# Kernel tuning notes

Measured on AMD Instinct MI355X. Metric: run time of the kernel, lower is better.

Reference implementation:

```python
import jax, jax.numpy as jnp
import numpy as np

T = 1024      # tokens
H = 2048      # hidden_size
I = 1408      # moe_intermediate_size
E = 16        # n_routed_experts
K = 6         # num_experts_per_tok
SI = I * 2    # shared experts intermediate (n_shared_experts=2)


def setup_inputs() -> dict:
    key = jax.random.key(0)
    ks = jax.random.split(key, 8)
    s = 0.02
    return {
        "x": jax.random.normal(ks[0], (T, H), jnp.float32),
        "gate_w": jax.random.normal(ks[1], (E, H), jnp.float32) * s,
        "w_gate": jax.random.normal(ks[2], (E, I, H), jnp.float32) * s,
        "w_up": jax.random.normal(ks[3], (E, I, H), jnp.float32) * s,
        "w_down": jax.random.normal(ks[4], (E, H, I), jnp.float32) * s,
        "sw_gate": jax.random.normal(ks[5], (SI, H), jnp.float32) * s,
        "sw_up": jax.random.normal(ks[6], (SI, H), jnp.float32) * s,
        "sw_down": jax.random.normal(ks[7], (H, SI), jnp.float32) * s,
    }


def reference(x, gate_w, w_gate, w_up, w_down, sw_gate, sw_up, sw_down):
    t = x.shape[0]
    # ---- router: softmax over experts, top-k, renormalize (norm_topk_prob) ----
    logits = x @ gate_w.T                                   # [T, E]
    probs = jax.nn.softmax(logits.astype(jnp.float32), axis=-1)
    topw, topi = jax.lax.top_k(probs, K)                    # [T, K]
    topw = topw / jnp.sum(topw, axis=-1, keepdims=True)
    # per-token per-expert combine weight (0 for unselected experts)
    comb = jnp.zeros((t, E), probs.dtype).at[
        jnp.arange(t)[:, None], topi
    ].add(topw)                                             # [T, E]

    # ---- routed experts: SwiGLU MLP per expert, weighted combine ----
    g = jnp.einsum('th,eih->tei', x, w_gate)                # [T, E, I]
    u = jnp.einsum('th,eih->tei', x, w_up)                  # [T, E, I]
    h = jax.nn.silu(g) * u                                  # [T, E, I]
    routed = jnp.einsum('te,tei,ehi->th', comb, h, w_down)  # [T, H]

    # ---- shared experts (always-on SwiGLU MLP) ----
    shared = (jax.nn.silu(x @ sw_gate.T) * (x @ sw_up.T)) @ sw_down.T  # [T, H]

    return routed + shared
```

## Files before the change

### kernel.cpp

```cpp
#include <hip/hip_runtime.h>
#include <stdint.h>

#define T_TOK 1024
#define H_DIM 2048
#define I_DIM 1408
#define E_NUM 16
#define K_TOP 6
#define SI_DIM 2816
#define PADCAP 8192

typedef __attribute__((ext_vector_type(8))) short short8;
typedef __attribute__((ext_vector_type(8))) unsigned short ushort8;
typedef __attribute__((ext_vector_type(4))) float f32x4;

__device__ __forceinline__ unsigned short f2b(float f) {
    unsigned u = __float_as_uint(f);
    u += 0x7fffu + ((u >> 16) & 1u);
    return (unsigned short)(u >> 16);
}
__device__ __forceinline__ float b2f(unsigned short s) {
    return __uint_as_float((unsigned)s << 16);
}

__device__ __forceinline__ int xcd_swizzle(int bid, int nwg) {
    const int q = nwg >> 3, r = nwg & 7;
    const int xcd = bid & 7, k = bid >> 3;
    const int base = (xcd < r) ? xcd * (q + 1) : r * (q + 1) + (xcd - r) * q;
    return base + k;
}

__global__ __launch_bounds__(256) void router_kernel(
    const float* __restrict__ x, const float* __restrict__ gw,
    float* __restrict__ topw, int* __restrict__ eidx, int* __restrict__ slotarr,
    int* __restrict__ counts)
{
    const int t = blockIdx.x, tid = threadIdx.x;
    const int lane = tid & 63, wave = tid >> 6;
    float part[E_NUM];
#pragma unroll
    for (int e = 0; e < E_NUM; ++e) part[e] = 0.f;
    const float* xr = x + (size_t)t * H_DIM;
    for (int i = tid; i < H_DIM; i += 256) {
        float xv = xr[i];
#pragma unroll
        for (int e = 0; e < E_NUM; ++e) part[e] += xv * gw[e * H_DIM + i];
    }
    __shared__ float red[4][E_NUM];
#pragma unroll
    for (int e = 0; e < E_NUM; ++e) {
        float v = part[e];
        for (int off = 32; off; off >>= 1) v += __shfl_down(v, off);
        if (lane == 0) red[wave][e] = v;
    }
    __syncthreads();
    if (tid == 0) {
        float logits[E_NUM];
#pragma unroll
        for (int e = 0; e < E_NUM; ++e)
            logits[e] = red[0][e] + red[1][e] + red[2][e] + red[3][e];
        int sel[K_TOP]; float selv[K_TOP];
        unsigned used = 0;
        for (int k = 0; k < K_TOP; ++k) {
            int best = 0; float bv = -1e30f;
            for (int e = 0; e < E_NUM; ++e)
                if (!((used >> e) & 1u) && logits[e] > bv) { bv = logits[e]; best = e; }
            used |= 1u << best; sel[k] = best; selv[k] = bv;
        }
        float mx = selv[0], s = 0.f, w[K_TOP];
        for (int k = 0; k < K_TOP; ++k) { w[k] = expf(selv[k] - mx); s += w[k]; }
        float inv = 1.f / s;
        for (int k = 0; k < K_TOP; ++k) {
            int slot = atomicAdd(&counts[sel[k]], 1);
            topw[t * K_TOP + k] = w[k] * inv;
            eidx[t * K_TOP + k] = sel[k];
            slotarr[t * K_TOP + k] = slot;
        }
    }
}

__global__ void zero_counts_kernel(int* counts) {
    if (threadIdx.x < E_NUM) counts[threadIdx.x] = 0;
}

__global__ void prefix_kernel(const int* __restrict__ counts, int* __restrict__ offs) {
    if (threadIdx.x == 0) {
        int o = 0;
        for (int e = 0; e < E_NUM; ++e) { offs[e] = o; o += (counts[e] + 127) & ~127; }
        offs[E_NUM] = o;
    }
}

__global__ __launch_bounds__(256) void gather_rows_kernel(
    const float* __restrict__ x, const int* __restrict__ eidx,
    const int* __restrict__ slotarr, const int* __restrict__ offs,
    ushort* __restrict__ Xg)
{
    const int b = blockIdx.x;
    const int t = b / K_TOP;
    const int e = eidx[b], s = slotarr[b];
    const size_t row = (size_t)offs[e] + (size_t)s;
    const float* src = x + (size_t)t * H_DIM;
    ushort* dst = Xg + row * H_DIM;
    const int i = threadIdx.x * 8;
    float4 f0 = *(const float4*)(src + i);
    float4 f1 = *(const float4*)(src + i + 4);
    ushort8 v;
    v[0] = f2b(f0.x); v[1] = f2b(f0.y); v[2] = f2b(f0.z); v[3] = f2b(f0.w);
    v[4] = f2b(f1.x); v[5] = f2b(f1.y); v[6] = f2b(f1.z); v[7] = f2b(f1.w);
    *(ushort8*)(dst + i) = v;
}

__global__ __launch_bounds__(256) void cvt_rows_kernel(
    const float* __restrict__ x, ushort* __restrict__ Xb)
{
    const size_t row = blockIdx.x;
    const float* src = x + row * H_DIM;
    ushort* dst = Xb + row * H_DIM;
    const int i = threadIdx.x * 8;
    float4 f0 = *(const float4*)(src + i);
    float4 f1 = *(const float4*)(src + i + 4);
    ushort8 v;
    v[0] = f2b(f0.x); v[1] = f2b(f0.y); v[2] = f2b(f0.z); v[3] = f2b(f0.w);
    v[4] = f2b(f1.x); v[5] = f2b(f1.y); v[6] = f2b(f1.z); v[7] = f2b(f1.w);
    *(ushort8*)(dst + i) = v;
}

template<int STORE_F32>
__global__ __launch_bounds__(256) void gemm_bt_kernel(
    const ushort* __restrict__ Abase,
    const float* __restrict__ B1, const float* __restrict__ B2,
    void* __restrict__ C1, void* __restrict__ C2,
    const int* __restrict__ counts, const int* __restrict__ offs,
    int Mconst, int nNT, int totNT, int nMT, int K, long strideB, int ldc)
{
    __shared__ short Alds[2][128 * 64];
    __shared__ short Blds[2][128 * 64];

    const int work = xcd_swizzle(blockIdx.x, gridDim.x);
    const int perE = totNT * nMT;
    const int e = work / perE;
    int rem = work - e * perE;
    int nt = rem / nMT;
    const int mt = rem - nt * nMT;

    int M = Mconst, rowbase = 0;
    if (counts) { M = counts[e]; rowbase = offs[e]; }
    const int row0 = mt * 128;
    if (row0 >= M) return;

    const float* Bsel = B1;
    void* Csel = C1;
    if (nt >= nNT) { Bsel = B2; Csel = C2; nt -= nNT; }
    const int n0 = nt * 128;
    const float* __restrict__ B = Bsel + (size_t)e * (size_t)strideB;
    const short* __restrict__ A = (const short*)Abase + (size_t)(rowbase + row0) * K;

    const int tid = threadIdx.x;
    const int lane = tid & 63;
    const int wave = tid >> 6;
    const int wm = wave & 1, wn = wave >> 1;
    const int l15 = lane & 15, lhi = lane >> 4;

    const int r0 = tid >> 3, sl = tid & 7;
    const int swsl = sl ^ (r0 & 7);
    const int ldsoff = (r0 << 6) + (swsl << 3);
    const short* Ag = A + (size_t)r0 * K + (sl << 3);
    const float* Bg = B + (size_t)(n0 + r0) * K + (sl << 3);

    f32x4 acc[4][4];
#pragma unroll
    for (int m = 0; m < 4; ++m)
#pragma unroll
        for (int n = 0; n < 4; ++n) acc[m][n] = (f32x4){0.f, 0.f, 0.f, 0.f};

    short8 a_reg[4];
    float4 b_reg[4][2];

    auto issue = [&](int k0) {
#pragma unroll
        for (int i = 0; i < 4; ++i) {
            a_reg[i] = *(const short8*)(Ag + (size_t)(i << 5) * K + k0);
            const float* bp = Bg + (size_t)(i << 5) * K + k0;
            b_reg[i][0] = *(const float4*)bp;
            b_reg[i][1] = *(const float4*)(bp + 4);
        }
    };
    auto store_lds = [&](int p) {
#pragma unroll
        for (int i = 0; i < 4; ++i) {
            const int off = ldsoff + (i << 11);
            *(short8*)&Alds[p][off] = a_reg[i];
            short8 v;
            v[0] = (short)f2b(b_reg[i][0].x); v[1] = (short)f2b(b_reg[i][0].y);
            v[2] = (short)f2b(b_reg[i][0].z); v[3] = (short)f2b(b_reg[i][0].w);
            v[4] = (short)f2b(b_reg[i][1].x); v[5] = (short)f2b(b_reg[i][1].y);
            v[6] = (short)f2b(b_reg[i][1].z); v[7] = (short)f2b(b_reg[i][1].w);
            *(short8*)&Blds[p][off] = v;
        }
    };

    const int nK = K >> 6;
    issue(0);
    store_lds(0);
    __syncthreads();

    int p = 0;
    for (int t = 0; t < nK; ++t) {
        const bool more = (t + 1 < nK);
        if (more) issue((t + 1) << 6);
#pragma unroll
        for (int kk = 0; kk < 2; ++kk) {
            short8 af[4], bfr[4];
            const int kb = (kk << 2) + lhi;
#pragma unroll
            for (int m = 0; m < 4; ++m) {
                const int rA = (wm << 6) + (m << 4) + l15;
                af[m] = *(const short8*)&Alds[p][(rA << 6) + ((kb ^ (rA & 7)) << 3)];
            }
#pragma unroll
            for (int n = 0; n < 4; ++n) {
                const int rB = (wn << 6) + (n << 4) + l15;
                bfr[n] = *(const short8*)&Blds[p][(rB << 6) + ((kb ^ (rB & 7)) << 3)];
            }
#pragma unroll
            for (int m = 0; m < 4; ++m)
#pragma unroll
                for (int n = 0; n < 4; ++n)
                    acc[m][n] = __builtin_amdgcn_mfma_f32_16x16x32_bf16(
                        af[m], bfr[n], acc[m][n], 0, 0, 0);
        }
        if (more) store_lds(p ^ 1);
        __syncthreads();
        p ^= 1;
    }

    const size_t cbase_col = (size_t)n0 + (wn << 6) + l15;
#pragma unroll
    for (int m = 0; m < 4; ++m) {
        const int rloc = (wm << 6) + (m << 4) + (lhi << 2);
#pragma unroll
        for (int j = 0; j < 4; ++j) {
            const int crow = row0 + rloc + j;
            if (crow >= M) continue;
            const size_t co = (size_t)(rowbase + crow) * ldc + cbase_col;
            if (STORE_F32) {
                float* C = (float*)Csel;
#pragma unroll
                for (int n = 0; n < 4; ++n) C[co + (n << 4)] = acc[m][n][j];
            } else {
                ushort* C = (ushort*)Csel;
#pragma unroll
                for (int n = 0; n < 4; ++n) C[co + (n << 4)] = f2b(acc[m][n][j]);
            }
        }
    }
}

__global__ __launch_bounds__(256) void silu_rows_kernel(
    const ushort* __restrict__ G, const ushort* __restrict__ U,
    ushort* __restrict__ Hh, const int* __restrict__ eidx,
    const int* __restrict__ slotarr, const int* __restrict__ offs, int rowlen)
{
    size_t row;
    if (eidx) {
        const int b = blockIdx.x;
        row = (size_t)offs[eidx[b]] + (size_t)slotarr[b];
    } else {
        row = blockIdx.x;
    }
    const ushort* g = G + row * rowlen;
    const ushort* u = U + row * rowlen;
    ushort* h = Hh + row * rowlen;
    for (int i = threadIdx.x * 8; i < rowlen; i += 2048) {
        ushort8 gv = *(const ushort8*)(g + i);
        ushort8 uv = *(const ushort8*)(u + i);
        ushort8 hv;
#pragma unroll
        for (int j = 0; j < 8; ++j) {
            float gf = b2f(gv[j]);
            float uf = b2f(uv[j]);
            float sf = gf / (1.f + expf(-gf));
            hv[j] = f2b(sf * uf);
        }
        *(ushort8*)(h + i) = hv;
    }
}

__global__ __launch_bounds__(256) void combine_kernel(
    float* __restrict__ out, const ushort* __restrict__ Y,
    const float* __restrict__ topw, const int* __restrict__ eidx,
    const int* __restrict__ slotarr, const int* __restrict__ offs)
{
    const int t = blockIdx.x;
    const int i = threadIdx.x * 8;
    float* o = out + (size_t)t * H_DIM;
    float acc[8];
    float4 o0 = *(const float4*)(o + i);
    float4 o1 = *(const float4*)(o + i + 4);
    acc[0] = o0.x; acc[1] = o0.y; acc[2] = o0.z; acc[3] = o0.w;
    acc[4] = o1.x; acc[5] = o1.y; acc[6] = o1.z; acc[7] = o1.w;
#pragma unroll
    for (int k = 0; k < K_TOP; ++k) {
        const float w = topw[t * K_TOP + k];
        const size_t row = (size_t)offs[eidx[t * K_TOP + k]] + (size_t)slotarr[t * K_TOP + k];
        ushort8 v = *(const ushort8*)(Y + row * H_DIM + i);
#pragma unroll
        for (int j = 0; j < 8; ++j) acc[j] += w * b2f(v[j]);
    }
    o0.x = acc[0]; o0.y = acc[1]; o0.z = acc[2]; o0.w = acc[3];
    o1.x = acc[4]; o1.y = acc[5]; o1.z = acc[6]; o1.w = acc[7];
    *(float4*)(o + i) = o0;
    *(float4*)(o + i + 4) = o1;
}

extern "C" void kernel_launch(void* const* d_in, const int* in_sizes, int n_in,
                              void* d_out, int out_size, void* d_ws, size_t ws_size,
                              hipStream_t stream) {
    const float* x       = (const float*)d_in[0];
    const float* gate_w  = (const float*)d_in[1];
    const float* w_gate  = (const float*)d_in[2];
    const float* w_up    = (const float*)d_in[3];
    const float* w_down  = (const float*)d_in[4];
    const float* sw_gate = (const float*)d_in[5];
    const float* sw_up   = (const float*)d_in[6];
    const float* sw_down = (const float*)d_in[7];
    float* out = (float*)d_out;

    char* p = (char*)d_ws;
    auto take = [&](size_t b) { char* r = p; p += (b + 255) & ~(size_t)255; return r; };
    int*    counts = (int*)take(E_NUM * 4);
    int*    offs   = (int*)take((E_NUM + 1) * 4);
    float*  topw   = (float*)take((size_t)T_TOK * K_TOP * 4);
    int*    eidx   = (int*)take((size_t)T_TOK * K_TOP * 4);
    int*    slot   = (int*)take((size_t)T_TOK * K_TOP * 4);
    ushort* Xg     = (ushort*)take((size_t)PADCAP * H_DIM * 2);
    ushort* G      = (ushort*)take((size_t)PADCAP * I_DIM * 2);
    ushort* U      = (ushort*)take((size_t)PADCAP * I_DIM * 2);
    ushort* Hr     = (ushort*)take((size_t)PADCAP * I_DIM * 2);
    ushort* Xb     = (ushort*)take((size_t)T_TOK * H_DIM * 2);
    ushort* Gs     = (ushort*)take((size_t)T_TOK * SI_DIM * 2);
    ushort* Us     = (ushort*)take((size_t)T_TOK * SI_DIM * 2);
    ushort* Hs     = (ushort*)take((size_t)T_TOK * SI_DIM * 2);

    zero_counts_kernel<<<1, 64, 0, stream>>>(counts);
    router_kernel<<<T_TOK, 256, 0, stream>>>(x, gate_w, topw, eidx, slot, counts);
    prefix_kernel<<<1, 64, 0, stream>>>(counts, offs);
    gather_rows_kernel<<<T_TOK * K_TOP, 256, 0, stream>>>(x, eidx, slot, offs, Xg);
    cvt_rows_kernel<<<T_TOK, 256, 0, stream>>>(x, Xb);

    gemm_bt_kernel<0><<<E_NUM * 22 * 8, 256, 0, stream>>>(
        Xg, w_gate, w_up, G, U, counts, offs,
        0, 11, 22, 8, H_DIM, (long)I_DIM * H_DIM, I_DIM);
    silu_rows_kernel<<<T_TOK * K_TOP, 256, 0, stream>>>(G, U, Hr, eidx, slot, offs, I_DIM);
    gemm_bt_kernel<0><<<E_NUM * 16 * 8, 256, 0, stream>>>(
        Hr, w_down, nullptr, Xg, nullptr, counts, offs,
        0, 16, 16, 8, I_DIM, (long)H_DIM * I_DIM, H_DIM);

    gemm_bt_kernel<0><<<44 * 8, 256, 0, stream>>>(
        Xb, sw_gate, sw_up, Gs, Us, nullptr, nullptr,
        T_TOK, 22, 44, 8, H_DIM, 0, SI_DIM);
    silu_rows_kernel<<<T_TOK, 256, 0, stream>>>(Gs, Us, Hs, nullptr, nullptr, nullptr, SI_DIM);
    gemm_bt_kernel<1><<<16 * 8, 256, 0, stream>>>(
        Hs, sw_down, nullptr, out, nullptr, nullptr, nullptr,
        T_TOK, 16, 16, 8, SI_DIM, 0, H_DIM);

    combine_kernel<<<T_TOK, 256, 0, stream>>>(out, Xg, topw, eidx, slot, offs);
}
```

Baseline: 511.3 us.

## Load GEMM tiles directly into LDS and convert fp32 weights at fragment read

Replaces the register-staged, double-buffered global-to-LDS copy with direct global_load_lds transfers into a single LDS buffer. The B operand is now kept in LDS as fp32 and converted to bf16 with packed cvt instructions when fragments are read, rather than being converted before the LDS store. This is meant to cut VGPR pressure and the instructions spent staging data through registers. The cost is losing overlap between loads and MFMA, since each k-step waits on barriers around the load, and B now uses twice the LDS bandwidth and is converted redundantly by every wave that reads it.

New measurement: 553.8 us, median of 2. 8.3% more time.

```diff
diff --git a/kernel.cpp b/kernel.cpp
--- a/kernel.cpp
+++ b/kernel.cpp
@@ -20,6 +20,18 @@
 }
 __device__ __forceinline__ float b2f(unsigned short s) {
     return __uint_as_float((unsigned)s << 16);
+}
+
+__device__ __forceinline__ unsigned cvt_pk2(float a, float b) {
+    unsigned r;
+    asm("v_cvt_pk_bf16_f32 %0, %1, %2" : "=v"(r) : "v"(a), "v"(b));
+    return r;
+}
+
+typedef __attribute__((address_space(1))) const unsigned int as1_uint;
+typedef __attribute__((address_space(3))) unsigned int as3_uint;
+__device__ __forceinline__ void gload16(const void* g, void* l) {
+    __builtin_amdgcn_global_load_lds((as1_uint*)g, (as3_uint*)l, 16, 0, 0);
 }
 
 __device__ __forceinline__ int xcd_swizzle(int bid, int nwg) {
@@ -133,8 +145,8 @@
     const int* __restrict__ counts, const int* __restrict__ offs,
     int Mconst, int nNT, int totNT, int nMT, int K, long strideB, int ldc)
 {
-    __shared__ short Alds[2][128 * 64];
-    __shared__ short Blds[2][128 * 64];
+    __shared__ short Alds[128 * 64];
+    __shared__ float Blds[128 * 64];
 
     const int work = xcd_swizzle(blockIdx.x, gridDim.x);
     const int perE = totNT * nMT;
@@ -153,7 +165,8 @@
     if (nt >= nNT) { Bsel = B2; Csel = C2; nt -= nNT; }
     const int n0 = nt * 128;
     const float* __restrict__ B = Bsel + (size_t)e * (size_t)strideB;
-    const short* __restrict__ A = (const short*)Abase + (size_t)(rowbase + row0) * K;
+    const char* __restrict__ Ab = (const char*)(Abase + (size_t)(rowbase + row0) * K);
+    const char* __restrict__ Bb = (const char*)(B + (size_t)n0 * K);
 
     const int tid = threadIdx.x;
     const int lane = tid & 63;
@@ -161,11 +174,26 @@
     const int wm = wave & 1, wn = wave >> 1;
     const int l15 = lane & 15, lhi = lane >> 4;
 
-    const int r0 = tid >> 3, sl = tid & 7;
-    const int swsl = sl ^ (r0 & 7);
-    const int ldsoff = (r0 << 6) + (swsl << 3);
-    const short* Ag = A + (size_t)r0 * K + (sl << 3);
-    const float* Bg = B + (size_t)(n0 + r0) * K + (sl << 3);
+    int aRow[4], aSlot[4];
+    char* aDst[4];
+#pragma unroll
+    for (int i = 0; i < 4; ++i) {
+        const int chunk = wave * 4 + i;
+        const int off = chunk * 1024 + lane * 16;
+        const int r = off >> 7, s = (off >> 4) & 7;
+        aRow[i] = r; aSlot[i] = s ^ (r & 7);
+        aDst[i] = (char*)Alds + chunk * 1024;
+    }
+    int bRow[8], bSlot[8];
+    char* bDst[8];
+#pragma unroll
+    for (int i = 0; i < 8; ++i) {
+        const int chunk = wave * 8 + i;
+        const int off = chunk * 1024 + lane * 16;
+        const int r = off >> 8, s = (off >> 4) & 15;
+        bRow[i] = r; bSlot[i] = s ^ (r & 7);
+        bDst[i] = (char*)Blds + chunk * 1024;
+    }
 
     f32x4 acc[4][4];
 #pragma unroll
@@ -173,54 +201,40 @@
 #pragma unroll
         for (int n = 0; n < 4; ++n) acc[m][n] = (f32x4){0.f, 0.f, 0.f, 0.f};
 
-    short8 a_reg[4];
-    float4 b_reg[4][2];
-
-    auto issue = [&](int k0) {
-#pragma unroll
-        for (int i = 0; i < 4; ++i) {
-            a_reg[i] = *(const short8*)(Ag + (size_t)(i << 5) * K + k0);
-            const float* bp = Bg + (size_t)(i << 5) * K + k0;
-            b_reg[i][0] = *(const float4*)bp;
-            b_reg[i][1] = *(const float4*)(bp + 4);
-        }
-    };
-    auto store_lds = [&](int p) {
-#pragma unroll
-        for (int i = 0; i < 4; ++i) {
-            const int off = ldsoff + (i << 11);
-            *(short8*)&Alds[p][off] = a_reg[i];
-            short8 v;
-            v[0] = (short)f2b(b_reg[i][0].x); v[1] = (short)f2b(b_reg[i][0].y);
-            v[2] = (short)f2b(b_reg[i][0].z); v[3] = (short)f2b(b_reg[i][0].w);
-            v[4] = (short)f2b(b_reg[i][1].x); v[5] = (short)f2b(b_reg[i][1].y);
-            v[6] = (short)f2b(b_reg[i][1].z); v[7] = (short)f2b(b_reg[i][1].w);
-            *(short8*)&Blds[p][off] = v;
-        }
-    };
-
     const int nK = K >> 6;
-    issue(0);
-    store_lds(0);
-    __syncthreads();
-
-    int p = 0;
-    for (int t = 0; t < nK; ++t) {
-        const bool more = (t + 1 < nK);
-        if (more) issue((t + 1) << 6);
+    for (int kt = 0; kt < nK; ++kt) {
+        const int k0 = kt << 6;
+        __syncthreads();
+#pragma unroll
+        for (int i = 0; i < 4; ++i)
+            gload16(Ab + (size_t)aRow[i] * K * 2 + k0 * 2 + (aSlot[i] << 4), aDst[i]);
+#pragma unroll
+        for (int i = 0; i < 8; ++i)
+            gload16(Bb + (size_t)bRow[i] * K * 4 + k0 * 4 + (bSlot[i] << 4), bDst[i]);
+        __syncthreads();
+
 #pragma unroll
         for (int kk = 0; kk < 2; ++kk) {
+            const int kb = (kk << 2) + lhi;
             short8 af[4], bfr[4];
-            const int kb = (kk << 2) + lhi;
 #pragma unroll
             for (int m = 0; m < 4; ++m) {
                 const int rA = (wm << 6) + (m << 4) + l15;
-                af[m] = *(const short8*)&Alds[p][(rA << 6) + ((kb ^ (rA & 7)) << 3)];
+                af[m] = *(const short8*)&Alds[(rA << 6) + ((kb ^ (rA & 7)) << 3)];
             }
 #pragma unroll
             for (int n = 0; n < 4; ++n) {
                 const int rB = (wn << 6) + (n << 4) + l15;
-                bfr[n] = *(const short8*)&Blds[p][(rB << 6) + ((kb ^ (rB & 7)) << 3)];
+                const int s0 = (kb << 1) ^ (rB & 7);
+                const int s1 = ((kb << 1) | 1) ^ (rB & 7);
+                f32x4 x0 = *(const f32x4*)&Blds[(rB << 6) + (s0 << 2)];
+                f32x4 x1 = *(const f32x4*)&Blds[(rB << 6) + (s1 << 2)];
+                union { short8 s8; unsigned u[4]; } bb;
+                bb.u[0] = cvt_pk2(x0[0], x0[1]);
+                bb.u[1] = cvt_pk2(x0[2], x0[3]);
+                bb.u[2] = cvt_pk2(x1[0], x1[1]);
+                bb.u[3] = cvt_pk2(x1[2], x1[3]);
+                bfr[n] = bb.s8;
             }
 #pragma unroll
             for (int m = 0; m < 4; ++m)
@@ -229,9 +243,6 @@
                     acc[m][n] = __builtin_amdgcn_mfma_f32_16x16x32_bf16(
                         af[m], bfr[n], acc[m][n], 0, 0, 0);
         }
-        if (more) store_lds(p ^ 1);
-        __syncthreads();
-        p ^= 1;
     }
 
     const size_t cbase_col = (size_t)n0 + (wn << 6) + l15;
```
